# Kernel optimization log

Measured on AMD Instinct MI355X. Metric: run time of the kernel, lower is better.

## Reference

```python
import jax, jax.numpy as jnp
import numpy as np

HEAD_SIZE = 64

def setup_inputs() -> dict:
    key = jax.random.key(0)
    k1, k2, k3, k4 = jax.random.split(key, 4)
    B, T, D = 4, 4096, 768
    x = jax.random.normal(k1, (B, T, D), dtype=jnp.float32)
    Wq = jax.random.normal(k2, (D, HEAD_SIZE), dtype=jnp.float32) * (1.0 / np.sqrt(D))
    Wk = jax.random.normal(k3, (D, HEAD_SIZE), dtype=jnp.float32) * (1.0 / np.sqrt(D))
    Wv = jax.random.normal(k4, (D, HEAD_SIZE), dtype=jnp.float32) * (1.0 / np.sqrt(D))
    return {"x": x, "Wq": Wq, "Wk": Wk, "Wv": Wv}

def reference(x, Wq, Wk, Wv):
    # q,k,v: [B, T, H]
    q = jnp.einsum('btd,dh->bth', x, Wq)
    k = jnp.einsum('btd,dh->bth', x, Wk)
    v = jnp.einsum('btd,dh->bth', x, Wv)
    # scores: [B, T, T]; causal mask via lower-triangular band, -inf elsewhere
    scores = jnp.einsum('bqh,bkh->bqk', q, k)
    T = x.shape[1]
    causal = jnp.tril(jnp.ones((T, T), dtype=bool))  # band_part(ones, -1, 0)
    scores = jnp.where(causal[None, :, :], scores, -jnp.inf)
    attn = jax.nn.softmax(scores / np.sqrt(HEAD_SIZE), axis=-1)
    # dropout is identity in eval mode
    return jnp.einsum('bqk,bkh->bqh', attn, v)
```

## Files before the change

kernel.cpp:

```cpp
#include <hip/hip_runtime.h>
#include <math.h>

typedef __attribute__((ext_vector_type(8))) short short8;
typedef __attribute__((ext_vector_type(4))) float f32x4;
typedef unsigned short ushort_t;

#define TSEQ   4096
#define NBATCH 4
#define DMODEL 768
#define HS     64
#define KSPLIT 4

static __device__ __forceinline__ ushort_t f2bf(float f) {
  union { float f; unsigned u; } v; v.f = f;
  unsigned r = v.u + 0x7fffu + ((v.u >> 16) & 1u);
  return (ushort_t)(r >> 16);
}
static __device__ __forceinline__ float bf2f(ushort_t u) {
  union { unsigned u; float f; } v; v.u = ((unsigned)u) << 16; return v.f;
}

#define MFMA16(a,b,c) __builtin_amdgcn_mfma_f32_16x16x32_bf16((a),(b),(c),0,0,0)

__global__ __launch_bounds__(256) void wprep(
    const float* __restrict__ Wq, const float* __restrict__ Wk,
    const float* __restrict__ Wv, ushort_t* __restrict__ Wt)
{
  __shared__ float lds[64 * 65];
  const int m = blockIdx.x / 12, kc = blockIdx.x % 12, k0 = kc * 64;
  const float* W = (m == 0) ? Wq : (m == 1) ? Wk : Wv;
  const int tid = threadIdx.x;
#pragma unroll
  for (int i = 0; i < 16; i++) {
    const int row = i * 4 + (tid >> 6), col = tid & 63;
    lds[row * 65 + col] = W[(size_t)(k0 + row) * HS + col];
  }
  __syncthreads();
#pragma unroll
  for (int i = 0; i < 16; i++) {
    const int n = i * 4 + (tid >> 6), kk = tid & 63;
    Wt[(size_t)(m * 64 + n) * DMODEL + k0 + kk] = f2bf(lds[kk * 65 + n]);
  }
}

__global__ __launch_bounds__(256, 2) void qkv_mfma(
    const float* __restrict__ x, const ushort_t* __restrict__ Wt,
    ushort_t* __restrict__ q, ushort_t* __restrict__ kO, ushort_t* __restrict__ vT)
{
  __shared__ __align__(16) ushort_t sA[2][32 * 72];
  __shared__ __align__(16) ushort_t sB[2][192 * 64];

  const int tid  = threadIdx.x;
  const int w    = tid >> 6;
  const int lane = tid & 63;
  const int l16  = lane & 15, quad = lane >> 4;
  const int M0   = blockIdx.x * 32;

  const int arow = tid >> 3, acol = (tid & 7) * 8;
  const float* ax = x + (size_t)(M0 + arow) * DMODEL + acol;

  const int bcol_l = lane >> 3;
  const int bkoff  = (((lane & 7) ^ (bcol_l & 7)) << 3);

  f32x4 acc[2][3];
#pragma unroll
  for (int mt = 0; mt < 2; mt++)
#pragma unroll
    for (int nt = 0; nt < 3; nt++) acc[mt][nt] = (f32x4){0.f, 0.f, 0.f, 0.f};

  {
#pragma unroll
    for (int j = 0; j < 6; j++) {
      const int colb = w * 48 + j * 8;
      __builtin_amdgcn_global_load_lds(
          (const __attribute__((address_space(1))) ushort_t*)
              (Wt + (size_t)(colb + bcol_l) * DMODEL + bkoff),
          (__attribute__((address_space(3))) ushort_t*)(&sB[0][colb * 64]),
          16, 0, 0);
    }
    const float4 f0 = *(const float4*)(ax);
    const float4 f1 = *(const float4*)(ax + 4);
    short8 p;
    p[0]=f2bf(f0.x); p[1]=f2bf(f0.y); p[2]=f2bf(f0.z); p[3]=f2bf(f0.w);
    p[4]=f2bf(f1.x); p[5]=f2bf(f1.y); p[6]=f2bf(f1.z); p[7]=f2bf(f1.w);
    *(short8*)(&sA[0][arow * 72 + acol]) = p;
  }

  for (int ks = 0; ks < DMODEL / 64; ks++) {
    const int cur = ks & 1, nxt = cur ^ 1;
    __syncthreads();

    float4 f0n, f1n;
    if (ks < DMODEL / 64 - 1) {
#pragma unroll
      for (int j = 0; j < 6; j++) {
        const int colb = w * 48 + j * 8;
        __builtin_amdgcn_global_load_lds(
            (const __attribute__((address_space(1))) ushort_t*)
                (Wt + (size_t)(colb + bcol_l) * DMODEL + (ks + 1) * 64 + bkoff),
            (__attribute__((address_space(3))) ushort_t*)(&sB[nxt][colb * 64]),
            16, 0, 0);
      }
      f0n = *(const float4*)(ax + (ks + 1) * 64);
      f1n = *(const float4*)(ax + (ks + 1) * 64 + 4);
    }

    const ushort_t* sAc = &sA[cur][0];
    const ushort_t* sBc = &sB[cur][0];
#pragma unroll
    for (int kc = 0; kc < 2; kc++) {
      const short8 a0 = *(const short8*)(sAc + (l16)      * 72 + kc * 32 + quad * 8);
      const short8 a1 = *(const short8*)(sAc + (16 + l16) * 72 + kc * 32 + quad * 8);
      const int kswz = (kc * 32 + quad * 8) ^ ((l16 & 7) << 3);
#pragma unroll
      for (int nt = 0; nt < 3; nt++) {
        const short8 bf =
            *(const short8*)(sBc + (w * 48 + nt * 16 + l16) * 64 + kswz);
        acc[0][nt] = MFMA16(a0, bf, acc[0][nt]);
        acc[1][nt] = MFMA16(a1, bf, acc[1][nt]);
      }
    }

    if (ks < DMODEL / 64 - 1) {
      short8 p;
      p[0]=f2bf(f0n.x); p[1]=f2bf(f0n.y); p[2]=f2bf(f0n.z); p[3]=f2bf(f0n.w);
      p[4]=f2bf(f1n.x); p[5]=f2bf(f1n.y); p[6]=f2bf(f1n.z); p[7]=f2bf(f1n.w);
      *(short8*)(&sA[nxt][arow * 72 + acol]) = p;
    }
  }

#pragma unroll
  for (int mt = 0; mt < 2; mt++)
#pragma unroll
    for (int nt = 0; nt < 3; nt++) {
      const int gnt = w * 3 + nt;
      const int mat = gnt >> 2;
      if (mat == 0) {
        const int col = (gnt & 3) * 16 + l16;
#pragma unroll
        for (int r = 0; r < 4; r++)
          q[(size_t)(M0 + mt * 16 + quad * 4 + r) * HS + col] =
              f2bf(acc[mt][nt][r] * 0.125f);
      } else if (mat == 1) {
        const int cb2 = (gnt & 3) * 2 + (l16 >> 3);
#pragma unroll
        for (int r = 0; r < 4; r++) {
          const int trow  = M0 + mt * 16 + quad * 4 + r;
          const int cphys = ((cb2 ^ (trow & 7)) << 3) | (l16 & 7);
          kO[(size_t)trow * HS + cphys] = f2bf(acc[mt][nt][r]);
        }
      }
    }
  __syncthreads();
  float* vls = (float*)&sA[0][0];
#pragma unroll
  for (int mt = 0; mt < 2; mt++)
#pragma unroll
    for (int nt = 0; nt < 3; nt++) {
      const int gnt = w * 3 + nt;
      if ((gnt >> 2) == 2) {
        const int vcol = (gnt & 3) * 16 + l16;
#pragma unroll
        for (int r = 0; r < 4; r++)
          vls[(mt * 16 + quad * 4 + r) * 65 + vcol] = acc[mt][nt][r];
      }
    }
  __syncthreads();
  const int d = tid >> 2, seg = tid & 3;
  short8 pk;
#pragma unroll
  for (int i = 0; i < 8; i++) pk[i] = (short)f2bf(vls[(seg * 8 + i) * 65 + d]);
  {
    const int t0  = M0 & (TSEQ - 1);
    const int tb  = t0 & ~63;
    const int kb  = ((t0 & 63) >> 3) + seg;
    const int kbp = kb ^ (d & 7);
    *(short8*)(vT + ((size_t)(M0 >> 12) * HS + d) * TSEQ + tb + kbp * 8) = pk;
  }
}

#define KP 72
__global__ __launch_bounds__(256, 3) void attn_part(
    const ushort_t* __restrict__ q, const ushort_t* __restrict__ k,
    const ushort_t* __restrict__ vT, float* __restrict__ ML, ushort_t* __restrict__ OP)
{
  __shared__ __align__(16) ushort_t sK[2][64 * 64];
  __shared__ __align__(16) ushort_t sV[2][64 * 64];
  __shared__ __align__(16) ushort_t sP[4][16 * KP];

  const int idx  = blockIdx.x;
  const int s    = idx & 3;
  const int b    = (idx >> 2) & 3;
  const int jt   = 63 - (idx >> 4);
  const int tid  = threadIdx.x;
  const int w    = tid >> 6;
  const int lane = tid & 63;
  const int l16  = lane & 15, quad = lane >> 4;
  const int R0   = jt * 64 + w * 16;

  const ushort_t* qg = q  + (size_t)b * TSEQ * HS;
  const ushort_t* kg = k  + (size_t)b * TSEQ * HS;
  const ushort_t* vg = vT + (size_t)b * HS * TSEQ;

  const short8 qf0 = *(const short8*)(qg + (size_t)(R0 + l16) * HS +      quad * 8);
  const short8 qf1 = *(const short8*)(qg + (size_t)(R0 + l16) * HS + 32 + quad * 8);

  f32x4 o[4];
#pragma unroll
  for (int dt = 0; dt < 4; dt++) o[dt] = (f32x4){0.f, 0.f, 0.f, 0.f};
  float mrow = -INFINITY, lrow = 0.f;

  const int nkt = jt + 1;
  const int srow = lane >> 3;
  const int scol = (lane & 7) * 8;

  int kt = s, cur = 0;
  if (kt < nkt) {
    const int k0 = kt * 64;
#pragma unroll
    for (int j = 0; j < 2; j++) {
      const int r0 = w * 16 + j * 8;
      __builtin_amdgcn_global_load_lds(
          (const __attribute__((address_space(1))) ushort_t*)
              (kg + (size_t)(k0 + r0 + srow) * HS + scol),
          (__attribute__((address_space(3))) ushort_t*)(&sK[0][r0 * 64]),
          16, 0, 0);
      __builtin_amdgcn_global_load_lds(
          (const __attribute__((address_space(1))) ushort_t*)
              (vg + (size_t)(r0 + srow) * TSEQ + k0 + scol),
          (__attribute__((address_space(3))) ushort_t*)(&sV[0][r0 * 64]),
          16, 0, 0);
    }
  }
  for (; kt < nkt; kt += KSPLIT) {
    const int k0 = kt * 64;
    __syncthreads();
    if (kt + KSPLIT < nkt) {
      const int kn = (kt + KSPLIT) * 64;
#pragma unroll
      for (int j = 0; j < 2; j++) {
        const int r0 = w * 16 + j * 8;
        __builtin_amdgcn_global_load_lds(
            (const __attribute__((address_space(1))) ushort_t*)
                (kg + (size_t)(kn + r0 + srow) * HS + scol),
            (__attribute__((address_space(3))) ushort_t*)(&sK[cur ^ 1][r0 * 64]),
            16, 0, 0);
        __builtin_amdgcn_global_load_lds(
            (const __attribute__((address_space(1))) ushort_t*)
                (vg + (size_t)(r0 + srow) * TSEQ + kn + scol),
            (__attribute__((address_space(3))) ushort_t*)(&sV[cur ^ 1][r0 * 64]),
            16, 0, 0);
      }
    }
    const ushort_t* sKc = &sK[cur][0];
    const ushort_t* sVc = &sV[cur][0];
    const int sw = (l16 & 7) << 3;

    f32x4 sT[4];
#pragma unroll
    for (int ct = 0; ct < 4; ct++) {
      sT[ct] = (f32x4){0.f, 0.f, 0.f, 0.f};
      const short8 kfa = *(const short8*)(sKc + (ct * 16 + l16) * 64 + ((quad * 8)      ^ sw));
      const short8 kfb = *(const short8*)(sKc + (ct * 16 + l16) * 64 + ((32 + quad * 8) ^ sw));
      sT[ct] = MFMA16(kfa, qf0, sT[ct]);
      sT[ct] = MFMA16(kfb, qf1, sT[ct]);
    }
    if (k0 + 63 > R0) {
      const int qrow = R0 + l16;
#pragma unroll
      for (int ct = 0; ct < 4; ct++)
#pragma unroll
        for (int r = 0; r < 4; r++)
          sT[ct][r] = (k0 + ct * 16 + quad * 4 + r <= qrow) ? sT[ct][r] : -INFINITY;
    }
    float tm = -INFINITY;
#pragma unroll
    for (int ct = 0; ct < 4; ct++)
#pragma unroll
      for (int r = 0; r < 4; r++) tm = fmaxf(tm, sT[ct][r]);
    tm = fmaxf(tm, __shfl_xor(tm, 16));
    tm = fmaxf(tm, __shfl_xor(tm, 32));
    const float mn = fmaxf(mrow, tm);
    const float al = __expf(mrow - mn);
    mrow = mn;
    float ps = 0.f;
#pragma unroll
    for (int ct = 0; ct < 4; ct++)
#pragma unroll
      for (int r = 0; r < 4; r++) { sT[ct][r] = __expf(sT[ct][r] - mn); ps += sT[ct][r]; }
    ps += __shfl_xor(ps, 16);
    ps += __shfl_xor(ps, 32);
    lrow = lrow * al + ps;
    ushort_t* Pw = &sP[w][0];
#pragma unroll
    for (int ct = 0; ct < 4; ct++) {
      ushort4 pk;
      pk.x = f2bf(sT[ct][0]); pk.y = f2bf(sT[ct][1]);
      pk.z = f2bf(sT[ct][2]); pk.w = f2bf(sT[ct][3]);
      *(ushort4*)(Pw + l16 * KP + ct * 16 + quad * 4) = pk;
    }
    float alo[4];
#pragma unroll
    for (int r = 0; r < 4; r++) alo[r] = __shfl(al, quad * 4 + r);
#pragma unroll
    for (int dt = 0; dt < 4; dt++)
#pragma unroll
      for (int r = 0; r < 4; r++) o[dt][r] *= alo[r];
    const short8 pf0 = *(const short8*)(Pw + l16 * KP +      quad * 8);
    const short8 pf1 = *(const short8*)(Pw + l16 * KP + 32 + quad * 8);
#pragma unroll
    for (int dt = 0; dt < 4; dt++) {
      const short8 vfa = *(const short8*)(sVc + (dt * 16 + l16) * 64 + ((quad * 8)      ^ sw));
      const short8 vfb = *(const short8*)(sVc + (dt * 16 + l16) * 64 + ((32 + quad * 8) ^ sw));
      o[dt] = MFMA16(pf0, vfa, o[dt]);
      o[dt] = MFMA16(pf1, vfb, o[dt]);
    }
    cur ^= 1;
  }

  const size_t base = ((size_t)(b * KSPLIT + s) * TSEQ);
  if (quad == 0) {
    ML[(base + R0 + l16) * 2 + 0] = mrow;
    ML[(base + R0 + l16) * 2 + 1] = lrow;
  }
#pragma unroll
  for (int dt = 0; dt < 4; dt++)
#pragma unroll
    for (int r = 0; r < 4; r++)
      OP[(base + R0 + quad * 4 + r) * HS + dt * 16 + l16] = f2bf(o[dt][r]);
}

__global__ __launch_bounds__(256) void attn_merge(
    const float* __restrict__ ML, const ushort_t* __restrict__ OP,
    float* __restrict__ out)
{
  const int row = blockIdx.x * 16 + (threadIdx.x >> 4);
  const int b   = row >> 12, t = row & (TSEQ - 1);
  const int d0  = (threadIdx.x & 15) * 4;
  float m[KSPLIT], l[KSPLIT];
  float M = -INFINITY;
#pragma unroll
  for (int ss = 0; ss < KSPLIT; ss++) {
    const size_t i = ((size_t)(b * KSPLIT + ss) * TSEQ + t);
    m[ss] = ML[i * 2]; l[ss] = ML[i * 2 + 1];
    M = fmaxf(M, m[ss]);
  }
  float den = 0.f;
  float4 num = make_float4(0.f, 0.f, 0.f, 0.f);
#pragma unroll
  for (int ss = 0; ss < KSPLIT; ss++) {
    const float a = __expf(m[ss] - M);
    den += l[ss] * a;
    const size_t i = ((size_t)(b * KSPLIT + ss) * TSEQ + t);
    const ushort4 u = *(const ushort4*)(OP + i * HS + d0);
    num.x += a * bf2f(u.x); num.y += a * bf2f(u.y);
    num.z += a * bf2f(u.z); num.w += a * bf2f(u.w);
  }
  const float inv = 1.f / den;
  *(float4*)(out + (size_t)row * HS + d0) =
      make_float4(num.x * inv, num.y * inv, num.z * inv, num.w * inv);
}

extern "C" void kernel_launch(void* const* d_in, const int* in_sizes, int n_in,
                              void* d_out, int out_size, void* d_ws, size_t ws_size,
                              hipStream_t stream) {
  const float* x  = (const float*)d_in[0];
  const float* Wq = (const float*)d_in[1];
  const float* Wk = (const float*)d_in[2];
  const float* Wv = (const float*)d_in[3];
  float* out = (float*)d_out;

  char* ws = (char*)d_ws;
  ushort_t* Wt = (ushort_t*)ws;
  ushort_t* qb = (ushort_t*)(ws + 294912);
  ushort_t* kb = (ushort_t*)(ws + 294912 + 2097152);
  ushort_t* vb = (ushort_t*)(ws + 294912 + 2 * 2097152);
  float*    ml = (float*)   (ws + 294912 + 3 * 2097152);
  ushort_t* op = (ushort_t*)(ws + 294912 + 3 * 2097152 + 524288);

  wprep<<<36, 256, 0, stream>>>(Wq, Wk, Wv, Wt);
  qkv_mfma<<<(NBATCH * TSEQ) / 32, 256, 0, stream>>>(x, Wt, qb, kb, vb);
  attn_part<<<64 * NBATCH * KSPLIT, 256, 0, stream>>>(qb, kb, vb, ml, op);
  attn_merge<<<1024, 256, 0, stream>>>(ml, op, out);
}
```

Baseline: 128.0 us.

## Fuse split-K merge into attention via atomic counter; swizzle P tile, add setprio

Removes the separate attn_merge launch. Each attention block bumps a per-(batch, query-tile) atomic counter, and the last of the KSPLIT blocks reads the partial m/l/O values and writes the final output. The counter is reset inside wprep. It also replaces the padded P buffer in LDS with an XOR-swizzled unpadded layout to cut LDS use, raises the occupancy hint from 3 to 4 blocks, and wraps the MFMA sections in s_setprio. The cost is threadfence overhead and a serialized merge tail in the last block of each tile.

New measurement: 327.6 us. 156% more time.

```diff
diff --git a/kernel.cpp b/kernel.cpp
--- a/kernel.cpp
+++ b/kernel.cpp
@@ -24,12 +24,13 @@
 
 __global__ __launch_bounds__(256) void wprep(
     const float* __restrict__ Wq, const float* __restrict__ Wk,
-    const float* __restrict__ Wv, ushort_t* __restrict__ Wt)
+    const float* __restrict__ Wv, ushort_t* __restrict__ Wt, int* __restrict__ cnt)
 {
   __shared__ float lds[64 * 65];
+  const int tid = threadIdx.x;
+  if (blockIdx.x == 0) cnt[tid] = 0;
   const int m = blockIdx.x / 12, kc = blockIdx.x % 12, k0 = kc * 64;
   const float* W = (m == 0) ? Wq : (m == 1) ? Wk : Wv;
-  const int tid = threadIdx.x;
 #pragma unroll
   for (int i = 0; i < 16; i++) {
     const int row = i * 4 + (tid >> 6), col = tid & 63;
@@ -179,14 +180,15 @@
   }
 }
 
-#define KP 72
-__global__ __launch_bounds__(256, 3) void attn_part(
+__global__ __launch_bounds__(256, 4) void attn_part(
     const ushort_t* __restrict__ q, const ushort_t* __restrict__ k,
-    const ushort_t* __restrict__ vT, float* __restrict__ ML, ushort_t* __restrict__ OP)
+    const ushort_t* __restrict__ vT, float* __restrict__ ML,
+    ushort_t* __restrict__ OP, int* __restrict__ cnt, float* __restrict__ out)
 {
   __shared__ __align__(16) ushort_t sK[2][64 * 64];
   __shared__ __align__(16) ushort_t sV[2][64 * 64];
-  __shared__ __align__(16) ushort_t sP[4][16 * KP];
+  __shared__ __align__(16) ushort_t sP[4][16 * 64];
+  __shared__ int sOld;
 
   const int idx  = blockIdx.x;
   const int s    = idx & 3;
@@ -257,6 +259,7 @@
     const int sw = (l16 & 7) << 3;
 
     f32x4 sT[4];
+    __builtin_amdgcn_s_setprio(1);
 #pragma unroll
     for (int ct = 0; ct < 4; ct++) {
       sT[ct] = (f32x4){0.f, 0.f, 0.f, 0.f};
@@ -265,6 +268,7 @@
       sT[ct] = MFMA16(kfa, qf0, sT[ct]);
       sT[ct] = MFMA16(kfb, qf1, sT[ct]);
     }
+    __builtin_amdgcn_s_setprio(0);
     if (k0 + 63 > R0) {
       const int qrow = R0 + l16;
 #pragma unroll
@@ -297,7 +301,8 @@
       ushort4 pk;
       pk.x = f2bf(sT[ct][0]); pk.y = f2bf(sT[ct][1]);
       pk.z = f2bf(sT[ct][2]); pk.w = f2bf(sT[ct][3]);
-      *(ushort4*)(Pw + l16 * KP + ct * 16 + quad * 4) = pk;
+      const int pb = (ct * 2 + (quad >> 1)) ^ (l16 & 7);
+      *(ushort4*)(Pw + l16 * 64 + pb * 8 + (quad & 1) * 4) = pk;
     }
     float alo[4];
 #pragma unroll
@@ -306,8 +311,9 @@
     for (int dt = 0; dt < 4; dt++)
 #pragma unroll
       for (int r = 0; r < 4; r++) o[dt][r] *= alo[r];
-    const short8 pf0 = *(const short8*)(Pw + l16 * KP +      quad * 8);
-    const short8 pf1 = *(const short8*)(Pw + l16 * KP + 32 + quad * 8);
+    const short8 pf0 = *(const short8*)(Pw + l16 * 64 + (((quad)     ^ (l16 & 7)) << 3));
+    const short8 pf1 = *(const short8*)(Pw + l16 * 64 + (((4 + quad) ^ (l16 & 7)) << 3));
+    __builtin_amdgcn_s_setprio(1);
 #pragma unroll
     for (int dt = 0; dt < 4; dt++) {
       const short8 vfa = *(const short8*)(sVc + (dt * 16 + l16) * 64 + ((quad * 8)      ^ sw));
@@ -315,6 +321,7 @@
       o[dt] = MFMA16(pf0, vfa, o[dt]);
       o[dt] = MFMA16(pf1, vfb, o[dt]);
     }
+    __builtin_amdgcn_s_setprio(0);
     cur ^= 1;
   }
 
@@ -328,37 +335,46 @@
 #pragma unroll
     for (int r = 0; r < 4; r++)
       OP[(base + R0 + quad * 4 + r) * HS + dt * 16 + l16] = f2bf(o[dt][r]);
-}
-
-__global__ __launch_bounds__(256) void attn_merge(
-    const float* __restrict__ ML, const ushort_t* __restrict__ OP,
-    float* __restrict__ out)
-{
-  const int row = blockIdx.x * 16 + (threadIdx.x >> 4);
-  const int b   = row >> 12, t = row & (TSEQ - 1);
-  const int d0  = (threadIdx.x & 15) * 4;
-  float m[KSPLIT], l[KSPLIT];
-  float M = -INFINITY;
-#pragma unroll
-  for (int ss = 0; ss < KSPLIT; ss++) {
-    const size_t i = ((size_t)(b * KSPLIT + ss) * TSEQ + t);
-    m[ss] = ML[i * 2]; l[ss] = ML[i * 2 + 1];
-    M = fmaxf(M, m[ss]);
-  }
-  float den = 0.f;
-  float4 num = make_float4(0.f, 0.f, 0.f, 0.f);
-#pragma unroll
-  for (int ss = 0; ss < KSPLIT; ss++) {
-    const float a = __expf(m[ss] - M);
-    den += l[ss] * a;
-    const size_t i = ((size_t)(b * KSPLIT + ss) * TSEQ + t);
-    const ushort4 u = *(const ushort4*)(OP + i * HS + d0);
-    num.x += a * bf2f(u.x); num.y += a * bf2f(u.y);
-    num.z += a * bf2f(u.z); num.w += a * bf2f(u.w);
-  }
-  const float inv = 1.f / den;
-  *(float4*)(out + (size_t)row * HS + d0) =
-      make_float4(num.x * inv, num.y * inv, num.z * inv, num.w * inv);
+
+  __threadfence();
+  if (tid == 0) sOld = atomicAdd(&cnt[b * 64 + jt], 1);
+  __syncthreads();
+  if (sOld == KSPLIT - 1) {
+    __threadfence();
+    const int rr = tid >> 2, d0 = (tid & 3) * 16;
+    const int row = jt * 64 + rr;
+    float m4[KSPLIT], l4[KSPLIT];
+    float M = -INFINITY;
+#pragma unroll
+    for (int ss = 0; ss < KSPLIT; ss++) {
+      const size_t i = ((size_t)(b * KSPLIT + ss) * TSEQ + row);
+      m4[ss] = ML[i * 2]; l4[ss] = ML[i * 2 + 1];
+      M = fmaxf(M, m4[ss]);
+    }
+    float den = 0.f;
+    float n0 = 0.f, n1 = 0.f, n2 = 0.f, n3 = 0.f, n4 = 0.f, n5 = 0.f, n6 = 0.f, n7 = 0.f;
+    float n8 = 0.f, n9 = 0.f, nA = 0.f, nB = 0.f, nC = 0.f, nD = 0.f, nE = 0.f, nF = 0.f;
+#pragma unroll
+    for (int ss = 0; ss < KSPLIT; ss++) {
+      const float a = __expf(m4[ss] - M);
+      den += l4[ss] * a;
+      const size_t i = ((size_t)(b * KSPLIT + ss) * TSEQ + row);
+      const ushort4 u0 = *(const ushort4*)(OP + i * HS + d0);
+      const ushort4 u1 = *(const ushort4*)(OP + i * HS + d0 + 4);
+      const ushort4 u2 = *(const ushort4*)(OP + i * HS + d0 + 8);
+      const ushort4 u3 = *(const ushort4*)(OP + i * HS + d0 + 12);
+      n0 += a * bf2f(u0.x); n1 += a * bf2f(u0.y); n2 += a * bf2f(u0.z); n3 += a * bf2f(u0.w);
+      n4 += a * bf2f(u1.x); n5 += a * bf2f(u1.y); n6 += a * bf2f(u1.z); n7 += a * bf2f(u1.w);
+      n8 += a * bf2f(u2.x); n9 += a * bf2f(u2.y); nA += a * bf2f(u2.z); nB += a * bf2f(u2.w);
+      nC += a * bf2f(u3.x); nD += a * bf2f(u3.y); nE += a * bf2f(u3.z); nF += a * bf2f(u3.w);
+    }
+    const float inv = 1.f / den;
+    float* op = out + ((size_t)(b * TSEQ + row)) * HS + d0;
+    *(float4*)(op)      = make_float4(n0 * inv, n1 * inv, n2 * inv, n3 * inv);
+    *(float4*)(op + 4)  = make_float4(n4 * inv, n5 * inv, n6 * inv, n7 * inv);
+    *(float4*)(op + 8)  = make_float4(n8 * inv, n9 * inv, nA * inv, nB * inv);
+    *(float4*)(op + 12) = make_float4(nC * inv, nD * inv, nE * inv, nF * inv);
+  }
 }
 
 extern "C" void kernel_launch(void* const* d_in, const int* in_sizes, int n_in,
@@ -377,9 +393,9 @@
   ushort_t* vb = (ushort_t*)(ws + 294912 + 2 * 2097152);
   float*    ml = (float*)   (ws + 294912 + 3 * 2097152);
   ushort_t* op = (ushort_t*)(ws + 294912 + 3 * 2097152 + 524288);
-
-  wprep<<<36, 256, 0, stream>>>(Wq, Wk, Wv, Wt);
+  int*      cn = (int*)     (ws + 294912 + 3 * 2097152 + 524288 + 8388608);
+
+  wprep<<<36, 256, 0, stream>>>(Wq, Wk, Wv, Wt, cn);
   qkv_mfma<<<(NBATCH * TSEQ) / 32, 256, 0, stream>>>(x, Wt, qb, kb, vb);
-  attn_part<<<64 * NBATCH * KSPLIT, 256, 0, stream>>>(qb, kb, vb, ml, op);
-  attn_merge<<<1024, 256, 0, stream>>>(ml, op, out);
-}
+  attn_part<<<64 * NBATCH * KSPLIT, 256, 0, stream>>>(qb, kb, vb, ml, op, cn, out);
+}
```
